# Optimization experiments

Hardware: AMD Instinct MI355X
Metric: run time of the kernel (lower is better)

Reference implementation:

```python
import jax, jax.numpy as jnp
import numpy as np

IN_DIM = 128
LAYER_DIMS = [128, 128]
NUM_SAMPLES = [25, 10]
L0 = 3072
NEG_WEIGHT = 1.0


def setup_inputs() -> dict:
    key = jax.random.key(0)
    ks = jax.random.split(key, 12)
    feat = jax.random.normal(ks[0], (L0, IN_DIM), dtype=jnp.float32)
    nodes = jax.random.randint(ks[1], (L0,), 0, L0)
    nb0 = jnp.arange(L0)
    nb1 = jax.random.randint(ks[2], (L0 * 10,), 0, L0)
    nb2 = jax.random.randint(ks[3], (L0 * 10 * 25,), 0, L0)
    src_idx = jax.random.randint(ks[4], (1024,), 0, L0)
    pos_idx = jax.random.randint(ks[5], (1024,), 0, L0)
    neg_idx = jax.random.randint(ks[6], (512,), 0, L0)
    g = 0.05
    # mean aggregator weights: layer0 in=IN_DIM, layer1 in=2*128 (concat)
    w_self_0 = jax.random.normal(ks[7], (IN_DIM, 128), jnp.float32) * g
    w_neigh_0 = jax.random.normal(ks[8], (IN_DIM, 128), jnp.float32) * g
    w_self_1 = jax.random.normal(ks[9], (256, 128), jnp.float32) * g
    w_neigh_1 = jax.random.normal(ks[10], (256, 128), jnp.float32) * g
    return dict(nodes=nodes, feat=feat, src_idx=src_idx, pos_idx=pos_idx,
                neg_idx=neg_idx, nb0=nb0, nb1=nb1, nb2=nb2,
                w_self_0=w_self_0, w_neigh_0=w_neigh_0,
                w_self_1=w_self_1, w_neigh_1=w_neigh_1)


def _aggregate(hidden, params):
    # GraphSAGE layer stack: at layer l, combine each hop with the mean of its
    # sampled neighbors, concat self/neigh transforms, relu except last layer.
    num_layers = len(NUM_SAMPLES)
    for layer in range(num_layers):
        w_self, w_neigh = params[layer]
        is_last = layer == num_layers - 1
        next_hidden = []
        for hop in range(num_layers - layer):
            s = NUM_SAMPLES[num_layers - hop - 1]
            self_v = hidden[hop]  # [n, d]
            neigh = hidden[hop + 1].reshape(self_v.shape[0], s, self_v.shape[1])
            neigh_mean = jnp.mean(neigh, axis=1)
            h = jnp.concatenate([self_v @ w_self, neigh_mean @ w_neigh], axis=1)
            if not is_last:
                h = jax.nn.relu(h)
            next_hidden.append(h)
        hidden = next_hidden
    return hidden[0]


def _l2_normalize(x, eps=1e-12):
    return x * jax.lax.rsqrt(jnp.maximum(jnp.sum(x * x, axis=1, keepdims=True), eps))


def reference(nodes, feat, src_idx, pos_idx, neg_idx, nb0, nb1, nb2,
              w_self_0, w_neigh_0, w_self_1, w_neigh_1):
    hidden = [feat[nb0], feat[nb1], feat[nb2]]
    params = [(w_self_0, w_neigh_0), (w_self_1, w_neigh_1)]
    output = _aggregate(hidden, params)          # [L0, 256]
    output = _l2_normalize(output)
    src_emb = output[src_idx]                    # [B, 256]
    pos_emb = output[pos_idx]
    neg_emb = output[neg_idx]                    # [Nneg, 256]

    aff = jnp.sum(src_emb * pos_emb, axis=1)     # [B]
    neg_aff = src_emb @ neg_emb.T                # [B, Nneg]

    # MRR via double argsort (tf double top_k equivalent; ties -> positive last)
    aff_all = jnp.concatenate([neg_aff, aff[:, None]], axis=1)
    order = jnp.argsort(-aff_all, axis=1, stable=True)
    ranks = jnp.argsort(order, axis=1, stable=True)
    mrr = jnp.mean(1.0 / (ranks[:, -1].astype(jnp.float32) + 1.0))

    # sigmoid cross-entropy: labels 1 -> softplus(-x); labels 0 -> softplus(x)
    true_xent = jax.nn.softplus(-aff)
    neg_xent = jax.nn.softplus(neg_aff)
    loss = jnp.sum(true_xent) + NEG_WEIGHT * jnp.sum(neg_xent)
    loss = loss / jnp.asarray(src_emb.shape[0], jnp.float32)
    return src_emb, loss, mrr
```

## Files before the change

kernel.cpp:

```cpp
#include <hip/hip_runtime.h>
#include <math.h>

#define L0      3072
#define DIM     128
#define BATCH   1024
#define NNEG    512


template<int K, int AW, int HOFF, bool NORM>
__global__ __launch_bounds__(256) void k_mm(
    const float* __restrict__ Ain,
    const float* __restrict__ W0, const float* __restrict__ W1,
    float* __restrict__ Out, const int ldo, const int outHalfOff) {
  __shared__ float AT[6 * AW];
  __shared__ float rs[4][3];
  const int t = threadIdx.x;
  const int base = blockIdx.x * 6;

  {
    const float4* __restrict__ src = (const float4*)(Ain + base * AW);
    float4* __restrict__ dst = (float4*)AT;
    const int n4 = 6 * AW / 4;
#pragma unroll
    for (int i = 0; i < n4; i += 256)
      if (i + t < n4) dst[i + t] = src[i + t];
  }
  __syncthreads();

  const int half = __builtin_amdgcn_readfirstlane(t >> 7);
  const int rg   = __builtin_amdgcn_readfirstlane(((t & 127) >> 6) * 3);
  const int c = t & 63;
  const float* __restrict__ W = (half ? W1 : W0) + c;
  const float* __restrict__ A0 = AT + rg * AW + half * HOFF;

  float acc[3][2];
#pragma unroll
  for (int r = 0; r < 3; ++r) { acc[r][0] = 0.f; acc[r][1] = 0.f; }

  float4 aC[3];
  float wC[8];
#pragma unroll
  for (int r = 0; r < 3; ++r) aC[r] = *(const float4*)&A0[r * AW];
#pragma unroll
  for (int i = 0; i < 4; ++i) {
    wC[i]     = W[i * 128];
    wC[4 + i] = W[i * 128 + 64];
  }
  for (int d = 0; d < K; d += 4) {
    const int dn = (d + 4 < K) ? d + 4 : 0;
    float4 aN[3];
    float wN[8];
#pragma unroll
    for (int r = 0; r < 3; ++r) aN[r] = *(const float4*)&A0[r * AW + dn];
#pragma unroll
    for (int i = 0; i < 4; ++i) {
      wN[i]     = W[(dn + i) * 128];
      wN[4 + i] = W[(dn + i) * 128 + 64];
    }
#pragma unroll
    for (int i = 0; i < 4; ++i)
#pragma unroll
      for (int r = 0; r < 3; ++r) {
        const float av = ((const float*)&aC[r])[i];
        acc[r][0] = fmaf(av, wC[i],     acc[r][0]);
        acc[r][1] = fmaf(av, wC[4 + i], acc[r][1]);
      }
#pragma unroll
    for (int r = 0; r < 3; ++r) aC[r] = aN[r];
#pragma unroll
    for (int i = 0; i < 8; ++i) wC[i] = wN[i];
  }

  float scale[3] = {1.f, 1.f, 1.f};
  if (NORM) {
    float p[3];
#pragma unroll
    for (int r = 0; r < 3; ++r) p[r] = acc[r][0] * acc[r][0] + acc[r][1] * acc[r][1];
#pragma unroll
    for (int off = 32; off > 0; off >>= 1)
#pragma unroll
      for (int r = 0; r < 3; ++r) p[r] += __shfl_xor(p[r], off, 64);
    const int wv = t >> 6;
    if ((t & 63) == 0) { rs[wv][0] = p[0]; rs[wv][1] = p[1]; rs[wv][2] = p[2]; }
    __syncthreads();
#pragma unroll
    for (int r = 0; r < 3; ++r) {
      const float s = (rg == 0) ? (rs[0][r] + rs[2][r]) : (rs[1][r] + rs[3][r]);
      scale[r] = rsqrtf(fmaxf(s, 1e-12f));
    }
  }
  float* __restrict__ O = Out + half * outHalfOff + c;
#pragma unroll
  for (int r = 0; r < 3; ++r) {
    O[(base + rg + r) * ldo]      = acc[r][0] * scale[r];
    O[(base + rg + r) * ldo + 64] = acc[r][1] * scale[r];
  }
}

__global__ __launch_bounds__(640) void k_aggregate(
    const float* __restrict__ X0, const float* __restrict__ Y0,
    const int* __restrict__ nb0, const int* __restrict__ nb1,
    const int* __restrict__ nb2, float* __restrict__ H) {
  __shared__ float sB[5][128], sC[5][128], sD[5][128];
  const int i = blockIdx.x;
  const int t = threadIdx.x;
  const int c = t & 127;
  const int g = __builtin_amdgcn_readfirstlane(t >> 7);

  float accB = 0.f, accC = 0.f, accD = 0.f;
#pragma unroll
  for (int jj = 0; jj < 2; ++jj) {
    const int j = g * 2 + jj;
    const int r = i * 10 + j;
    const int* __restrict__ p = nb2 + r * 25;
    float s = 0.f;
#pragma unroll
    for (int k = 0; k < 25; ++k) s += Y0[p[k] * 128 + c];
    accD += fmaxf(s * 0.04f, 0.f);
    const int r1 = nb1[r];
    accB += Y0[r1 * 128 + c];
    accC += fmaxf(X0[r1 * 128 + c], 0.f);
  }
  sB[g][c] = accB; sC[g][c] = accC; sD[g][c] = accD;
  __syncthreads();

  if (t < 512) {
    const int q = t >> 7;
    float v;
    if (q == 0) {
      v = fmaxf(X0[nb0[i] * 128 + c], 0.f);
    } else {
      const float (*S)[128] = (q == 1) ? sB : (q == 2) ? sC : sD;
      float s = S[0][c] + S[1][c] + S[2][c] + S[3][c] + S[4][c];
      v = (q == 1) ? fmaxf(s * 0.1f, 0.f) : s * 0.1f;
    }
    H[i * 512 + t] = v;
  }
}

__device__ __forceinline__ float softplusf(float x) {
  return fmaxf(x, 0.f) + log1pf(expf(-fabsf(x)));
}

__global__ __launch_bounds__(64) void k_aff(
    const float* __restrict__ O, const int* __restrict__ src_idx,
    const int* __restrict__ pos_idx, float* __restrict__ aff,
    float* __restrict__ spPos) {
  const int b = blockIdx.x * 64 + threadIdx.x;
  const float* __restrict__ ps = O + src_idx[b] * 256;
  const float* __restrict__ pp = O + pos_idx[b] * 256;
  float a = 0.f;
#pragma unroll 8
  for (int d = 0; d < 256; ++d) a = fmaf(ps[d], pp[d], a);
  aff[b] = a;
  float sp = softplusf(-a);
#pragma unroll
  for (int off = 32; off > 0; off >>= 1) sp += __shfl_down(sp, off, 64);
  if (threadIdx.x == 0) atomicAdd(spPos, sp);
}

__global__ __launch_bounds__(256) void k_srccopy(
    const float* __restrict__ R, const int* __restrict__ src_idx,
    float* __restrict__ out) {
  const int idx = blockIdx.x * 256 + threadIdx.x;
  const int b = idx >> 6, q = idx & 63;
  ((float4*)out)[b * 64 + q] = ((const float4*)R)[src_idx[b] * 64 + q];
}

__global__ __launch_bounds__(256) void k_neg(
    const float* __restrict__ O, const int* __restrict__ src_idx,
    const int* __restrict__ neg_idx, const float* __restrict__ aff,
    int* __restrict__ rank, float* __restrict__ spNeg) {
  __shared__ float SL[32][129];
  __shared__ float NL[64][129];
  __shared__ float affL[32];
  __shared__ int cntL[32];
  const int t = threadIdx.x;
  const int rowBase = (blockIdx.x >> 3) * 32;
  const int colBase = (blockIdx.x & 7) * 64;
  if (t < 32) { affL[t] = aff[rowBase + t]; cntL[t] = 0; }
  const int ct = t & 31;
  const int rt = t >> 5;
  float acc[4][2];
#pragma unroll
  for (int k = 0; k < 4; ++k) { acc[k][0] = 0.f; acc[k][1] = 0.f; }
  for (int ch = 0; ch < 2; ++ch) {
    __syncthreads();
    for (int idx = t; idx < 32 * 128; idx += 256) {
      int r = idx >> 7, dd = idx & 127;
      SL[r][dd] = O[src_idx[rowBase + r] * 256 + ch * 128 + dd];
    }
    for (int idx = t; idx < 64 * 128; idx += 256) {
      int cpos = idx >> 7, dd = idx & 127;
      NL[cpos][dd] = O[neg_idx[colBase + cpos] * 256 + ch * 128 + dd];
    }
    __syncthreads();
    for (int dd = 0; dd < 128; ++dd) {
      float n0 = NL[ct][dd], n1 = NL[ct + 32][dd];
#pragma unroll
      for (int k = 0; k < 4; ++k) {
        float sv = SL[rt + 8 * k][dd];
        acc[k][0] = fmaf(sv, n0, acc[k][0]);
        acc[k][1] = fmaf(sv, n1, acc[k][1]);
      }
    }
  }
  float sp = 0.f;
#pragma unroll
  for (int k = 0; k < 4; ++k) {
    float a = affL[rt + 8 * k];
    int cnt = 0;
#pragma unroll
    for (int cc = 0; cc < 2; ++cc) {
      float v = acc[k][cc];
      sp += softplusf(v);
      cnt += (v >= a) ? 1 : 0;
    }
    if (cnt) atomicAdd(&cntL[rt + 8 * k], cnt);
  }
#pragma unroll
  for (int off = 32; off > 0; off >>= 1) sp += __shfl_down(sp, off, 64);
  if ((t & 63) == 0) atomicAdd(spNeg, sp);
  __syncthreads();
  if (t < 32) atomicAdd(&rank[rowBase + t], cntL[t]);
}

__global__ __launch_bounds__(256) void k_finalize(
    const int* __restrict__ rank, const float* __restrict__ spPos,
    const float* __restrict__ spNeg, float* __restrict__ out) {
  const int t = threadIdx.x;
  float s = 0.f;
  for (int i = t; i < BATCH; i += 256) s += 1.f / (float)(rank[i] + 1);
#pragma unroll
  for (int off = 32; off > 0; off >>= 1) s += __shfl_down(s, off, 64);
  __shared__ float wsum[4];
  if ((t & 63) == 0) wsum[t >> 6] = s;
  __syncthreads();
  if (t == 0) {
    float mrr = (wsum[0] + wsum[1] + wsum[2] + wsum[3]) * (1.f / 1024.f);
    float loss = (spPos[0] + spNeg[0]) * (1.f / 1024.f);
    out[BATCH * 256]     = loss;
    out[BATCH * 256 + 1] = mrr;
  }
}

extern "C" void kernel_launch(void* const* d_in, const int* in_sizes, int n_in,
                              void* d_out, int out_size, void* d_ws, size_t ws_size,
                              hipStream_t stream) {
  const float* feat   = (const float*)d_in[1];
  const int* src_idx  = (const int*)d_in[2];
  const int* pos_idx  = (const int*)d_in[3];
  const int* neg_idx  = (const int*)d_in[4];
  const int* nb0      = (const int*)d_in[5];
  const int* nb1      = (const int*)d_in[6];
  const int* nb2      = (const int*)d_in[7];
  const float* ws0    = (const float*)d_in[8];
  const float* wn0    = (const float*)d_in[9];
  const float* ws1    = (const float*)d_in[10];
  const float* wn1    = (const float*)d_in[11];

  float* wsf   = (float*)d_ws;
  float* X0    = wsf;
  float* Y0    = wsf + 393216;
  float* H     = wsf + 786432;
  float* R     = wsf + 2359296;
  float* aff   = wsf + 3145728;
  float* spPos = wsf + 3146752;
  float* spNeg = wsf + 3146753;
  int*   rank  = (int*)(wsf + 3146754);
  float* out   = (float*)d_out;

  hipMemsetAsync(spPos, 0, (2 + BATCH) * sizeof(float), stream);

  k_mm<128, 128, 0, false><<<L0 / 6, 256, 0, stream>>>(feat, ws0, wn0,
                                                       X0, 128, 393216);
  k_aggregate<<<L0, 640, 0, stream>>>(X0, Y0, nb0, nb1, nb2, H);
  k_mm<256, 512, 256, true><<<L0 / 6, 256, 0, stream>>>(H, ws1, wn1,
                                                        R, 256, 128);
  k_aff<<<BATCH / 64, 64, 0, stream>>>(R, src_idx, pos_idx, aff, spPos);
  k_srccopy<<<BATCH * 64 / 256, 256, 0, stream>>>(R, src_idx, out);
  k_neg<<<(BATCH / 32) * (NNEG / 64), 256, 0, stream>>>(R, src_idx, neg_idx, aff, rank, spNeg);
  k_finalize<<<1, 256, 0, stream>>>(rank, spPos, spNeg, out);
}
```

Baseline: 177.8 us.

## Store layer-0 outputs as bf16, restructure gather, fuse src copy into aff kernel

Layer-0 matmul outputs X0/Y0 are now written as bf16, which halves the bytes moved by the dominant 25-neighbor gather in the aggregation kernel. The gather is rewritten to stage indices in shared memory and use 16-byte vector loads with shuffle reductions. The src embedding copy is fused into the affinity kernel, and the memset is folded into the first matmul block, so two launches are removed. The matmul loses its manual software prefetch in favor of unroll pragmas. bf16 rounding of intermediates adds numerical error.

Result: slower. 182.7 us (+2.7%).

```diff
diff --git a/kernel.cpp b/kernel.cpp
--- a/kernel.cpp
+++ b/kernel.cpp
@@ -7,28 +7,36 @@
 #define NNEG    512
 
 
-template<int K, int AW, int HOFF, bool NORM>
+__device__ __forceinline__ float bf2f(unsigned short u) {
+  return __uint_as_float(((unsigned)u) << 16);
+}
+__device__ __forceinline__ void store_out(float v, float* p) { *p = v; }
+__device__ __forceinline__ void store_out(float v, unsigned short* p) {
+  unsigned x = __float_as_uint(v);
+  *p = (unsigned short)((x + 0x7fff + ((x >> 16) & 1)) >> 16);
+}
+
+template<int K, int AW, int HOFF, bool NORM, typename OutT>
 __global__ __launch_bounds__(256) void k_mm(
     const float* __restrict__ Ain,
     const float* __restrict__ W0, const float* __restrict__ W1,
-    float* __restrict__ Out, const int ldo, const int outHalfOff) {
+    OutT* __restrict__ Out, const int ldo, const int outHalfOff,
+    float* __restrict__ zbuf, const int zcount) {
   __shared__ float AT[6 * AW];
   __shared__ float rs[4][3];
   const int t = threadIdx.x;
+  if (zbuf != nullptr && blockIdx.x == 0)
+    for (int z = t; z < zcount; z += 256) zbuf[z] = 0.f;
   const int base = blockIdx.x * 6;
-
   {
     const float4* __restrict__ src = (const float4*)(Ain + base * AW);
     float4* __restrict__ dst = (float4*)AT;
-    const int n4 = 6 * AW / 4;
-#pragma unroll
-    for (int i = 0; i < n4; i += 256)
-      if (i + t < n4) dst[i + t] = src[i + t];
-  }
-  __syncthreads();
-
-  const int half = __builtin_amdgcn_readfirstlane(t >> 7);
-  const int rg   = __builtin_amdgcn_readfirstlane(((t & 127) >> 6) * 3);
+    for (int idx = t; idx < 6 * AW / 4; idx += 256) dst[idx] = src[idx];
+  }
+  __syncthreads();
+
+  const int half = t >> 7;
+  const int rg = ((t >> 6) & 1) * 3;
   const int c = t & 63;
   const float* __restrict__ W = (half ? W1 : W0) + c;
   const float* __restrict__ A0 = AT + rg * AW + half * HOFF;
@@ -37,38 +45,25 @@
 #pragma unroll
   for (int r = 0; r < 3; ++r) { acc[r][0] = 0.f; acc[r][1] = 0.f; }
 
-  float4 aC[3];
-  float wC[8];
-#pragma unroll
-  for (int r = 0; r < 3; ++r) aC[r] = *(const float4*)&A0[r * AW];
-#pragma unroll
-  for (int i = 0; i < 4; ++i) {
-    wC[i]     = W[i * 128];
-    wC[4 + i] = W[i * 128 + 64];
-  }
+#pragma unroll 4
   for (int d = 0; d < K; d += 4) {
-    const int dn = (d + 4 < K) ? d + 4 : 0;
-    float4 aN[3];
-    float wN[8];
-#pragma unroll
-    for (int r = 0; r < 3; ++r) aN[r] = *(const float4*)&A0[r * AW + dn];
-#pragma unroll
-    for (int i = 0; i < 4; ++i) {
-      wN[i]     = W[(dn + i) * 128];
-      wN[4 + i] = W[(dn + i) * 128 + 64];
-    }
-#pragma unroll
-    for (int i = 0; i < 4; ++i)
+    float4 a[3];
+#pragma unroll
+    for (int r = 0; r < 3; ++r) a[r] = *(const float4*)&A0[r * AW + d];
+    float w0[4], w1[4];
+#pragma unroll
+    for (int i2 = 0; i2 < 4; ++i2) {
+      w0[i2] = W[(d + i2) * 128];
+      w1[i2] = W[(d + i2) * 128 + 64];
+    }
+#pragma unroll
+    for (int i2 = 0; i2 < 4; ++i2)
 #pragma unroll
       for (int r = 0; r < 3; ++r) {
-        const float av = ((const float*)&aC[r])[i];
-        acc[r][0] = fmaf(av, wC[i],     acc[r][0]);
-        acc[r][1] = fmaf(av, wC[4 + i], acc[r][1]);
+        const float av = ((const float*)&a[r])[i2];
+        acc[r][0] = fmaf(av, w0[i2], acc[r][0]);
+        acc[r][1] = fmaf(av, w1[i2], acc[r][1]);
       }
-#pragma unroll
-    for (int r = 0; r < 3; ++r) aC[r] = aN[r];
-#pragma unroll
-    for (int i = 0; i < 8; ++i) wC[i] = wN[i];
   }
 
   float scale[3] = {1.f, 1.f, 1.f};
@@ -89,50 +84,79 @@
       scale[r] = rsqrtf(fmaxf(s, 1e-12f));
     }
   }
-  float* __restrict__ O = Out + half * outHalfOff + c;
+  OutT* __restrict__ O = Out + half * outHalfOff + c;
 #pragma unroll
   for (int r = 0; r < 3; ++r) {
-    O[(base + rg + r) * ldo]      = acc[r][0] * scale[r];
-    O[(base + rg + r) * ldo + 64] = acc[r][1] * scale[r];
+    store_out(acc[r][0] * scale[r], &O[(base + rg + r) * ldo]);
+    store_out(acc[r][1] * scale[r], &O[(base + rg + r) * ldo + 64]);
   }
 }
 
 __global__ __launch_bounds__(640) void k_aggregate(
-    const float* __restrict__ X0, const float* __restrict__ Y0,
+    const unsigned short* __restrict__ X0, const unsigned short* __restrict__ Y0,
     const int* __restrict__ nb0, const int* __restrict__ nb1,
     const int* __restrict__ nb2, float* __restrict__ H) {
-  __shared__ float sB[5][128], sC[5][128], sD[5][128];
+  __shared__ int idxs[260];
+  __shared__ float gB[10][128], gC[10][128], gD[10][128];
   const int i = blockIdx.x;
   const int t = threadIdx.x;
-  const int c = t & 127;
-  const int g = __builtin_amdgcn_readfirstlane(t >> 7);
-
-  float accB = 0.f, accC = 0.f, accD = 0.f;
-#pragma unroll
-  for (int jj = 0; jj < 2; ++jj) {
-    const int j = g * 2 + jj;
-    const int r = i * 10 + j;
-    const int* __restrict__ p = nb2 + r * 25;
-    float s = 0.f;
-#pragma unroll
-    for (int k = 0; k < 25; ++k) s += Y0[p[k] * 128 + c];
-    accD += fmaxf(s * 0.04f, 0.f);
-    const int r1 = nb1[r];
-    accB += Y0[r1 * 128 + c];
-    accC += fmaxf(X0[r1 * 128 + c], 0.f);
-  }
-  sB[g][c] = accB; sC[g][c] = accC; sD[g][c] = accD;
+  if (t < 250) idxs[t] = nb2[i * 250 + t];
+  else if (t < 260) idxs[t] = nb1[i * 10 + t - 250];
+  __syncthreads();
+
+  const int j = t >> 6;
+  const int lam = t & 63;
+  const int c8 = lam & 15;
+  const int sub = lam >> 4;
+  const int* __restrict__ pj = idxs + j * 25;
+
+  float d8[8];
+#pragma unroll
+  for (int e = 0; e < 8; ++e) d8[e] = 0.f;
+#pragma unroll
+  for (int m = 0; m < 7; ++m) {
+    const int k = sub + 4 * m;
+    if (k < 25) {
+      const int r = pj[k];
+      const float4 raw = *(const float4*)(Y0 + r * 128 + c8 * 8);
+      const unsigned short* u = (const unsigned short*)&raw;
+#pragma unroll
+      for (int e = 0; e < 8; ++e) d8[e] += bf2f(u[e]);
+    }
+  }
+#pragma unroll
+  for (int e = 0; e < 8; ++e) d8[e] += __shfl_xor(d8[e], 16, 64);
+#pragma unroll
+  for (int e = 0; e < 8; ++e) d8[e] += __shfl_xor(d8[e], 32, 64);
+
+  const int r1 = idxs[250 + j];
+  if (sub == 0) {
+#pragma unroll
+    for (int e = 0; e < 8; ++e) gD[j][c8 * 8 + e] = fmaxf(d8[e] * 0.04f, 0.f);
+    const float4 raw = *(const float4*)(Y0 + r1 * 128 + c8 * 8);
+    const unsigned short* u = (const unsigned short*)&raw;
+#pragma unroll
+    for (int e = 0; e < 8; ++e) gB[j][c8 * 8 + e] = bf2f(u[e]);
+  } else if (sub == 1) {
+    const float4 raw = *(const float4*)(X0 + r1 * 128 + c8 * 8);
+    const unsigned short* u = (const unsigned short*)&raw;
+#pragma unroll
+    for (int e = 0; e < 8; ++e) gC[j][c8 * 8 + e] = fmaxf(bf2f(u[e]), 0.f);
+  }
   __syncthreads();
 
   if (t < 512) {
-    const int q = t >> 7;
+    const int q = t >> 7, c = t & 127;
     float v;
     if (q == 0) {
-      v = fmaxf(X0[nb0[i] * 128 + c], 0.f);
+      v = fmaxf(bf2f(X0[nb0[i] * 128 + c]), 0.f);
     } else {
-      const float (*S)[128] = (q == 1) ? sB : (q == 2) ? sC : sD;
-      float s = S[0][c] + S[1][c] + S[2][c] + S[3][c] + S[4][c];
-      v = (q == 1) ? fmaxf(s * 0.1f, 0.f) : s * 0.1f;
+      const float* g = (q == 1) ? &gB[0][0] : (q == 2) ? &gC[0][0] : &gD[0][0];
+      float s = 0.f;
+#pragma unroll
+      for (int jj = 0; jj < 10; ++jj) s += g[jj * 128 + c];
+      v = s * 0.1f;
+      if (q == 1) v = fmaxf(v, 0.f);
     }
     H[i * 512 + t] = v;
   }
@@ -144,27 +168,27 @@
 
 __global__ __launch_bounds__(64) void k_aff(
     const float* __restrict__ O, const int* __restrict__ src_idx,
-    const int* __restrict__ pos_idx, float* __restrict__ aff,
-    float* __restrict__ spPos) {
-  const int b = blockIdx.x * 64 + threadIdx.x;
-  const float* __restrict__ ps = O + src_idx[b] * 256;
-  const float* __restrict__ pp = O + pos_idx[b] * 256;
-  float a = 0.f;
-#pragma unroll 8
-  for (int d = 0; d < 256; ++d) a = fmaf(ps[d], pp[d], a);
-  aff[b] = a;
-  float sp = softplusf(-a);
-#pragma unroll
-  for (int off = 32; off > 0; off >>= 1) sp += __shfl_down(sp, off, 64);
-  if (threadIdx.x == 0) atomicAdd(spPos, sp);
-}
-
-__global__ __launch_bounds__(256) void k_srccopy(
-    const float* __restrict__ R, const int* __restrict__ src_idx,
-    float* __restrict__ out) {
-  const int idx = blockIdx.x * 256 + threadIdx.x;
-  const int b = idx >> 6, q = idx & 63;
-  ((float4*)out)[b * 64 + q] = ((const float4*)R)[src_idx[b] * 64 + q];
+    const int* __restrict__ pos_idx, float* __restrict__ out_src,
+    float* __restrict__ aff, float* __restrict__ spPos) {
+  __shared__ float4 sv[64], pv[64];
+  const int b = blockIdx.x;
+  const int q = threadIdx.x;
+  const int s = src_idx[b];
+  const int p = pos_idx[b];
+  float4 vs = ((const float4*)O)[s * 64 + q];
+  ((float4*)out_src)[b * 64 + q] = vs;
+  sv[q] = vs;
+  pv[q] = ((const float4*)O)[p * 64 + q];
+  __syncthreads();
+  if (q == 0) {
+    const float* __restrict__ ss = (const float*)sv;
+    const float* __restrict__ pp = (const float*)pv;
+    float a = 0.f;
+#pragma unroll 16
+    for (int d = 0; d < 256; ++d) a = fmaf(ss[d], pp[d], a);
+    aff[b] = a;
+    atomicAdd(spPos, softplusf(-a));
+  }
 }
 
 __global__ __launch_bounds__(256) void k_neg(
@@ -259,26 +283,23 @@
   const float* ws1    = (const float*)d_in[10];
   const float* wn1    = (const float*)d_in[11];
 
-  float* wsf   = (float*)d_ws;
-  float* X0    = wsf;
-  float* Y0    = wsf + 393216;
-  float* H     = wsf + 786432;
-  float* R     = wsf + 2359296;
-  float* aff   = wsf + 3145728;
-  float* spPos = wsf + 3146752;
-  float* spNeg = wsf + 3146753;
-  int*   rank  = (int*)(wsf + 3146754);
+  float* wsf = (float*)d_ws;
+  unsigned short* X0 = (unsigned short*)d_ws;
+  unsigned short* Y0 = X0 + 393216;
+  float* H     = wsf + 393216;
+  float* R     = wsf + 1966080;
+  float* aff   = wsf + 2752512;
+  float* spPos = wsf + 2753536;
+  float* spNeg = wsf + 2753537;
+  int*   rank  = (int*)(wsf + 2753538);
   float* out   = (float*)d_out;
 
-  hipMemsetAsync(spPos, 0, (2 + BATCH) * sizeof(float), stream);
-
-  k_mm<128, 128, 0, false><<<L0 / 6, 256, 0, stream>>>(feat, ws0, wn0,
-                                                       X0, 128, 393216);
+  k_mm<128, 128, 0, false, unsigned short><<<L0 / 6, 256, 0, stream>>>(
+      feat, ws0, wn0, X0, 128, 393216, spPos, 1026);
   k_aggregate<<<L0, 640, 0, stream>>>(X0, Y0, nb0, nb1, nb2, H);
-  k_mm<256, 512, 256, true><<<L0 / 6, 256, 0, stream>>>(H, ws1, wn1,
-                                                        R, 256, 128);
-  k_aff<<<BATCH / 64, 64, 0, stream>>>(R, src_idx, pos_idx, aff, spPos);
-  k_srccopy<<<BATCH * 64 / 256, 256, 0, stream>>>(R, src_idx, out);
+  k_mm<256, 512, 256, true, float><<<L0 / 6, 256, 0, stream>>>(
+      H, ws1, wn1, R, 256, 128, nullptr, 0);
+  k_aff<<<BATCH, 64, 0, stream>>>(R, src_idx, pos_idx, out, aff, spPos);
   k_neg<<<(BATCH / 32) * (NNEG / 64), 256, 0, stream>>>(R, src_idx, neg_idx, aff, rank, spNeg);
   k_finalize<<<1, 256, 0, stream>>>(rank, spPos, spNeg, out);
 }
```
